# Kernel optimization log

Measured on AMD Instinct MI355X. Metric: run time of the kernel, lower is better.

The kernel has to match this reference:

```python
import jax, jax.numpy as jnp
import numpy as np

N_NODES = 100000
N_EDGES = 3200000
IN_DIM = 128
HID = 64


def setup_inputs() -> dict:
    key = jax.random.key(0)
    ks = jax.random.split(key, 12)
    x = jax.random.normal(ks[0], (N_NODES, IN_DIM), dtype=jnp.float32)
    edge_index = jax.random.randint(ks[1], (2, N_EDGES), 0, N_NODES, dtype=jnp.int64)
    batch = jnp.zeros((N_NODES,), dtype=jnp.int64)
    s = 0.05
    params = {
        'fc_W': jax.random.normal(ks[2], (HID, IN_DIM), jnp.float32) * s,
        'fc_b': jnp.zeros((HID,), jnp.float32),
        # SAGEConv layer 1: lin_l (neighbor aggr, has bias), lin_r (root)
        'Wl1': jax.random.normal(ks[3], (HID, HID), jnp.float32) * s,
        'bl1': jnp.zeros((HID,), jnp.float32),
        'Wr1': jax.random.normal(ks[4], (HID, HID), jnp.float32) * s,
        # SAGEConv layer 2
        'Wl2': jax.random.normal(ks[5], (HID, HID), jnp.float32) * s,
        'bl2': jnp.zeros((HID,), jnp.float32),
        'Wr2': jax.random.normal(ks[6], (HID, HID), jnp.float32) * s,
        'head_W': jax.random.normal(ks[7], (1, HID), jnp.float32) * s,
        'head_b': jnp.zeros((1,), jnp.float32),
    }
    return {'x': x, 'edge_index': edge_index, 'batch': batch, **params}


def _sage_conv(h, src, dst, Wl, bl, Wr, n_nodes):
    # mean-aggregate neighbor features: gather over src, scatter-sum to dst
    msgs = h[src]                                            # [E, HID]
    agg = jax.ops.segment_sum(msgs, dst, num_segments=n_nodes)
    deg = jax.ops.segment_sum(jnp.ones((src.shape[0],), h.dtype), dst,
                              num_segments=n_nodes)
    agg = agg / jnp.maximum(deg, 1.0)[:, None]               # mean aggr
    return agg @ Wl.T + bl + h @ Wr.T                        # lin_l + lin_r


def reference(x, edge_index, batch, fc_W, fc_b, Wl1, bl1, Wr1, Wl2, bl2, Wr2,
              head_W, head_b):
    n_nodes = x.shape[0]
    src, dst = edge_index[0], edge_index[1]
    h = jax.nn.relu(x @ fc_W.T + fc_b)                       # fc + relu
    h = jax.nn.relu(_sage_conv(h, src, dst, Wl1, bl1, Wr1, n_nodes))  # SAGE 1 + relu
    h = _sage_conv(h, src, dst, Wl2, bl2, Wr2, n_nodes)      # SAGE 2 (no act)
    return h @ head_W.T + head_b                             # head -> [N, 1]
```

## Files before the change

### kernel.cpp

```cpp
#include <hip/hip_runtime.h>

#define N_NODES 100000
#define N_EDGES 3200000
#define IN_DIM 128
#define HID 64

#define NPB 32
#define NBUCK 3125
#define NBUCKP 3328
#define NBUCKP2 4096
#define TILE 12800
#define NSEG 250
#define RAWCAP 1408
#define FCB 391

typedef __attribute__((ext_vector_type(8))) short short8;
typedef __attribute__((ext_vector_type(4))) float f32x4;
typedef __attribute__((ext_vector_type(2))) float f32x2;

__device__ inline float bf2f(unsigned short u) {
    union { unsigned int u; float f; } c;
    c.u = ((unsigned int)u) << 16;
    return c.f;
}
__device__ inline unsigned short f2bf(float f) {
    union { float f; unsigned int u; } c;
    c.f = f;
    unsigned int u = c.u;
    return (unsigned short)((u + 0x7fffu + ((u >> 16) & 1u)) >> 16);
}
__device__ inline short8 cvt8(const float* __restrict__ p) {
    f32x4 lo = *reinterpret_cast<const f32x4*>(p);
    f32x4 hi = *reinterpret_cast<const f32x4*>(p + 4);
    short8 r;
#pragma unroll
    for (int j = 0; j < 4; ++j) { r[j] = (short)f2bf(lo[j]); r[4 + j] = (short)f2bf(hi[j]); }
    return r;
}
__device__ inline unsigned short pk_f8(float a, float b) {
    return (unsigned short)(__builtin_amdgcn_cvt_pk_fp8_f32(a, b, 0, false) & 0xffff);
}

__global__ __launch_bounds__(1024) void pre_kernel(
    const float* __restrict__ x, const float* __restrict__ fcW,
    const float* __restrict__ fcb, unsigned short* __restrict__ h0,
    unsigned char* __restrict__ h0f8,
    const int* __restrict__ ei, unsigned int* __restrict__ stage,
    int* __restrict__ offs,
    const float* __restrict__ Wl1, const float* __restrict__ Wr1,
    const float* __restrict__ Wl2, const float* __restrict__ Wr2,
    unsigned short* __restrict__ Wbf) {
    __shared__ int hoff[NBUCKP2];
    __shared__ int wsum[16];
    int tid = threadIdx.x;
    int lane = tid & 63, wid = tid >> 6;

    if (blockIdx.x < FCB) {
        int wtile = blockIdx.x * 16 + wid;
        if (wtile >= N_NODES / 16) return;
        int col = lane & 15, quad = lane >> 4;
        short8 bw[4][4];
#pragma unroll
        for (int nt = 0; nt < 4; ++nt)
#pragma unroll
            for (int ks = 0; ks < 4; ++ks)
                bw[nt][ks] = cvt8(fcW + (nt * 16 + col) * IN_DIM + ks * 32 + quad * 8);
        f32x4 acc[4];
#pragma unroll
        for (int nt = 0; nt < 4; ++nt) acc[nt] = {0.f, 0.f, 0.f, 0.f};
        int node0 = wtile * 16;
        const float* xrow = x + (size_t)(node0 + col) * IN_DIM + quad * 8;
#pragma unroll
        for (int ks = 0; ks < 4; ++ks) {
            short8 a = cvt8(xrow + ks * 32);
#pragma unroll
            for (int nt = 0; nt < 4; ++nt)
                acc[nt] = __builtin_amdgcn_mfma_f32_16x16x32_bf16(a, bw[nt][ks], acc[nt], 0, 0, 0);
        }
#pragma unroll
        for (int nt = 0; nt < 4; ++nt) {
            float bias = fcb[nt * 16 + col];
#pragma unroll
            for (int r = 0; r < 4; ++r) {
                float v = acc[nt][r] + bias;
                v = v > 0.f ? v : 0.f;
                int node = node0 + quad * 4 + r;
                int f = nt * 16 + col;
                h0[(size_t)node * HID + f] = f2bf(v);
                float w = __shfl_xor(v, 1);
                if (!(col & 1))
                    *(unsigned short*)(h0f8 + (size_t)node * HID + f) = pk_f8(v, w);
            }
        }
    } else if (blockIdx.x < FCB + NSEG) {
        int blk = blockIdx.x - FCB;
        int e0 = blk * TILE;
        int sd[13], ss[13];
        for (int i = tid; i < NBUCKP2; i += 1024) hoff[i] = 0;
        __syncthreads();
#pragma unroll
        for (int k = 0; k < 13; ++k) {
            int i = tid + k * 1024;
            if (i < TILE) {
                sd[k] = ei[(size_t)N_EDGES + e0 + i];
                ss[k] = ei[e0 + i];
                atomicAdd(&hoff[sd[k] >> 5], 1);
            }
        }
        __syncthreads();
        int base = tid * 4;
        int vals[4];
        int s = 0;
#pragma unroll
        for (int j = 0; j < 4; ++j) { vals[j] = s; s += hoff[base + j]; }
        int inc = s;
#pragma unroll
        for (int d = 1; d < 64; d <<= 1) {
            int n = __shfl_up(inc, d);
            if (lane >= d) inc += n;
        }
        int wave_excl = inc - s;
        if (lane == 63) wsum[wid] = inc;
        __syncthreads();
        if (tid == 0) {
            int r = 0;
#pragma unroll
            for (int w = 0; w < 16; ++w) { int t = wsum[w]; wsum[w] = r; r += t; }
        }
        __syncthreads();
        int tbase = wsum[wid] + wave_excl;
        __syncthreads();
#pragma unroll
        for (int j = 0; j < 4; ++j) hoff[base + j] = tbase + vals[j];
        __syncthreads();
        int* og = offs + (size_t)blk * NBUCKP;
        for (int i = tid; i < NBUCKP; i += 1024) og[i] = hoff[i];
        __syncthreads();
        unsigned int* sg = stage + (size_t)blk * TILE;
#pragma unroll
        for (int k = 0; k < 13; ++k) {
            int i = tid + k * 1024;
            if (i < TILE) {
                int pos = atomicAdd(&hoff[sd[k] >> 5], 1);
                sg[pos] = ((unsigned int)ss[k] << 5) | (unsigned int)(sd[k] & 31);
            }
        }
    } else {
        const float* mats[4] = {Wl1, Wr1, Wl2, Wr2};
#pragma unroll
        for (int m = 0; m < 4; ++m)
            for (int i = tid; i < HID * HID; i += 1024)
                Wbf[m * HID * HID + i] = f2bf(mats[m][i]);
    }
}

__global__ __launch_bounds__(256) void agg_sage(
    const unsigned short* __restrict__ h, const unsigned char* __restrict__ h8,
    const unsigned int* __restrict__ stage, const int* __restrict__ offs,
    unsigned int* __restrict__ g_srt, int* __restrict__ g_cnt,
    const unsigned short* __restrict__ Wlb, const unsigned short* __restrict__ Wrb,
    const float* __restrict__ bl, const float* __restrict__ hw,
    const float* __restrict__ hbias,
    unsigned short* __restrict__ h_out, unsigned char* __restrict__ h8_out,
    float* __restrict__ head_out, int do_head, int mode) {
    __shared__ unsigned int raw[RAWCAP];
    __shared__ unsigned int srt[RAWCAP];
    __shared__ unsigned int aggT[NPB][36];
    __shared__ int cnt32[NPB], off32[NPB], pos32[NPB];
    __shared__ int seg_alloc;
    __shared__ float headacc[NPB];
    int tid = threadIdx.x;
    int lane = tid & 63, wid = tid >> 6;
    int b = blockIdx.x;

    if (mode == 0) {
        if (tid == 0) seg_alloc = 0;
        if (tid < NPB) { cnt32[tid] = 0; headacc[tid] = 0.f; }
        __syncthreads();
        if (tid < NSEG) {
            const int* ob = offs + (size_t)tid * NBUCKP + b;
            int s2 = ob[0], e2 = ob[1];
            int n = e2 - s2;
            if (n > 0) {
                int p = atomicAdd(&seg_alloc, n);
                if (p + n > RAWCAP) n = (RAWCAP > p) ? (RAWCAP - p) : 0;
                const unsigned int* sp = stage + (size_t)tid * TILE + s2;
                for (int i = 0; i < n; ++i) raw[p + i] = sp[i];
            }
        }
        __syncthreads();
        int total = seg_alloc;
        if (total > RAWCAP) total = RAWCAP;
        for (int i = tid; i < total; i += 256) atomicAdd(&cnt32[raw[i] & 31], 1);
        __syncthreads();
        if (tid == 0) {
            int r = 0;
            for (int j = 0; j < NPB; ++j) { off32[j] = r; pos32[j] = r; r += cnt32[j]; }
        }
        __syncthreads();
        for (int i = tid; i < total; i += 256) {
            unsigned int u = raw[i];
            int p = atomicAdd(&pos32[u & 31], 1);
            srt[p] = u >> 5;
        }
        __syncthreads();
        for (int i = tid; i < total; i += 256) g_srt[(size_t)b * RAWCAP + i] = srt[i];
        if (tid < NPB) {
            g_cnt[b * 64 + tid] = cnt32[tid];
            g_cnt[b * 64 + 32 + tid] = off32[tid];
        }
    } else {
        if (tid < NPB) {
            cnt32[tid] = g_cnt[b * 64 + tid];
            off32[tid] = g_cnt[b * 64 + 32 + tid];
            headacc[tid] = 0.f;
        }
        __syncthreads();
        int total = off32[NPB - 1] + cnt32[NPB - 1];
        for (int i = tid; i < total; i += 256) srt[i] = g_srt[(size_t)b * RAWCAP + i];
        __syncthreads();
    }

    int q = lane >> 4, f4 = lane & 15;
#pragma unroll
    for (int k = 0; k < 8; ++k) {
        int d = wid * 8 + k;
        int s = off32[d], n = cnt32[d];
        float a0 = 0.f, a1 = 0.f, a2 = 0.f, a3 = 0.f;
        int i = 0;
        for (; i + 32 <= n; i += 32) {
            unsigned int g[8];
#pragma unroll
            for (int j = 0; j < 8; ++j) {
                unsigned int e = srt[s + i + j * 4 + q];
                g[j] = *(const unsigned int*)(h8 + (size_t)e * HID + f4 * 4);
            }
#pragma unroll
            for (int j = 0; j < 8; ++j) {
                f32x2 lo = __builtin_amdgcn_cvt_pk_f32_fp8(g[j], false);
                f32x2 hi = __builtin_amdgcn_cvt_pk_f32_fp8(g[j], true);
                a0 += lo.x; a1 += lo.y; a2 += hi.x; a3 += hi.y;
            }
        }
        for (; i + 16 <= n; i += 16) {
            unsigned int g[4];
#pragma unroll
            for (int j = 0; j < 4; ++j) {
                unsigned int e = srt[s + i + j * 4 + q];
                g[j] = *(const unsigned int*)(h8 + (size_t)e * HID + f4 * 4);
            }
#pragma unroll
            for (int j = 0; j < 4; ++j) {
                f32x2 lo = __builtin_amdgcn_cvt_pk_f32_fp8(g[j], false);
                f32x2 hi = __builtin_amdgcn_cvt_pk_f32_fp8(g[j], true);
                a0 += lo.x; a1 += lo.y; a2 += hi.x; a3 += hi.y;
            }
        }
        for (; i < n; i += 4) {
            int valid = (i + q) < n;
            unsigned int e = srt[valid ? (s + i + q) : s];
            unsigned int g = *(const unsigned int*)(h8 + (size_t)e * HID + f4 * 4);
            if (valid) {
                f32x2 lo = __builtin_amdgcn_cvt_pk_f32_fp8(g, false);
                f32x2 hi = __builtin_amdgcn_cvt_pk_f32_fp8(g, true);
                a0 += lo.x; a1 += lo.y; a2 += hi.x; a3 += hi.y;
            }
        }
        a0 += __shfl_xor(a0, 16); a0 += __shfl_xor(a0, 32);
        a1 += __shfl_xor(a1, 16); a1 += __shfl_xor(a1, 32);
        a2 += __shfl_xor(a2, 16); a2 += __shfl_xor(a2, 32);
        a3 += __shfl_xor(a3, 16); a3 += __shfl_xor(a3, 32);
        if (q == 0) {
            float inv = n > 0 ? 1.f / (float)n : 0.f;
            aggT[d][f4 * 2] = (unsigned int)f2bf(a0 * inv) |
                              ((unsigned int)f2bf(a1 * inv) << 16);
            aggT[d][f4 * 2 + 1] = (unsigned int)f2bf(a2 * inv) |
                                  ((unsigned int)f2bf(a3 * inv) << 16);
        }
    }
    __syncthreads();

    {
        int t = wid >> 1, np = wid & 1;
        int col = lane & 15, quad = lane >> 4;
        int m = t * 16 + col;
        int node0 = b * NPB;

        short8 aggA[2], hinA[2];
        const unsigned short* aggrow = (const unsigned short*)&aggT[m][0];
#pragma unroll
        for (int ks = 0; ks < 2; ++ks) {
            aggA[ks] = *reinterpret_cast<const short8*>(aggrow + ks * 32 + quad * 8);
            hinA[ks] = *reinterpret_cast<const short8*>(
                h + (size_t)(node0 + m) * HID + ks * 32 + quad * 8);
        }
        short8 bwl[2][2], bwr[2][2];
#pragma unroll
        for (int nt = 0; nt < 2; ++nt) {
            int f = np * 32 + nt * 16 + col;
#pragma unroll
            for (int ks = 0; ks < 2; ++ks) {
                bwl[nt][ks] = *reinterpret_cast<const short8*>(
                    Wlb + (size_t)f * HID + ks * 32 + quad * 8);
                bwr[nt][ks] = *reinterpret_cast<const short8*>(
                    Wrb + (size_t)f * HID + ks * 32 + quad * 8);
            }
        }
        f32x4 acc[2];
#pragma unroll
        for (int nt = 0; nt < 2; ++nt) acc[nt] = {0.f, 0.f, 0.f, 0.f};
#pragma unroll
        for (int ks = 0; ks < 2; ++ks) {
#pragma unroll
            for (int nt = 0; nt < 2; ++nt) {
                acc[nt] = __builtin_amdgcn_mfma_f32_16x16x32_bf16(aggA[ks], bwl[nt][ks], acc[nt], 0, 0, 0);
                acc[nt] = __builtin_amdgcn_mfma_f32_16x16x32_bf16(hinA[ks], bwr[nt][ks], acc[nt], 0, 0, 0);
            }
        }

        if (!do_head) {
#pragma unroll
            for (int nt = 0; nt < 2; ++nt) {
                int f = np * 32 + nt * 16 + col;
                float bias = bl[f];
#pragma unroll
                for (int r = 0; r < 4; ++r) {
                    float v = acc[nt][r] + bias;
                    v = v > 0.f ? v : 0.f;
                    int node = node0 + t * 16 + quad * 4 + r;
                    h_out[(size_t)node * HID + f] = f2bf(v);
                    float w = __shfl_xor(v, 1);
                    if (!(col & 1))
                        *(unsigned short*)(h8_out + (size_t)node * HID + f) = pk_f8(v, w);
                }
            }
        } else {
            float vr[4] = {0.f, 0.f, 0.f, 0.f};
#pragma unroll
            for (int nt = 0; nt < 2; ++nt) {
                int f = np * 32 + nt * 16 + col;
                float w = hw[f], bias = bl[f];
#pragma unroll
                for (int r = 0; r < 4; ++r) vr[r] += (acc[nt][r] + bias) * w;
            }
#pragma unroll
            for (int r = 0; r < 4; ++r) {
#pragma unroll
                for (int d = 1; d < 16; d <<= 1) vr[r] += __shfl_xor(vr[r], d);
            }
            if (col == 0) {
#pragma unroll
                for (int r = 0; r < 4; ++r)
                    atomicAdd(&headacc[t * 16 + quad * 4 + r], vr[r]);
            }
            __syncthreads();
            if (tid < NPB) head_out[node0 + tid] = headacc[tid] + hbias[0];
        }
    }
}

extern "C" void kernel_launch(void* const* d_in, const int* in_sizes, int n_in,
                              void* d_out, int out_size, void* d_ws, size_t ws_size,
                              hipStream_t stream) {
    const float* x   = (const float*)d_in[0];
    const int*   ei  = (const int*)d_in[1];
    const float* fcW = (const float*)d_in[3];
    const float* fcb = (const float*)d_in[4];
    const float* Wl1 = (const float*)d_in[5];
    const float* bl1 = (const float*)d_in[6];
    const float* Wr1 = (const float*)d_in[7];
    const float* Wl2 = (const float*)d_in[8];
    const float* bl2 = (const float*)d_in[9];
    const float* Wr2 = (const float*)d_in[10];
    const float* hW  = (const float*)d_in[11];
    const float* hb  = (const float*)d_in[12];
    float* out = (float*)d_out;

    char* ws = (char*)d_ws;
    size_t off = 0;
    auto alloc = [&](size_t bytes) -> char* {
        char* p = ws + off;
        off = (off + bytes + 255) & ~(size_t)255;
        return p;
    };
    unsigned short* h0   = (unsigned short*)alloc((size_t)N_NODES * HID * 2);
    unsigned short* h1   = (unsigned short*)alloc((size_t)N_NODES * HID * 2);
    unsigned char*  h0f8 = (unsigned char*)alloc((size_t)N_NODES * HID);
    unsigned char*  h1f8 = (unsigned char*)alloc((size_t)N_NODES * HID);
    unsigned int* stage  = (unsigned int*)alloc((size_t)N_EDGES * 4);
    int* offs            = (int*)alloc((size_t)NSEG * NBUCKP * 4);
    unsigned int* g_srt  = (unsigned int*)alloc((size_t)NBUCK * RAWCAP * 4);
    int* g_cnt           = (int*)alloc((size_t)NBUCK * 64 * 4);
    unsigned short* Wbf  = (unsigned short*)alloc((size_t)4 * HID * HID * 2);

    pre_kernel<<<FCB + NSEG + 1, 1024, 0, stream>>>(
        x, fcW, fcb, h0, h0f8, ei, stage, offs, Wl1, Wr1, Wl2, Wr2, Wbf);
    agg_sage<<<NBUCK, 256, 0, stream>>>(h0, h0f8, stage, offs, g_srt, g_cnt,
                                        Wbf, Wbf + HID * HID, bl1,
                                        nullptr, nullptr, h1, h1f8, nullptr, 0, 0);
    agg_sage<<<NBUCK, 256, 0, stream>>>(h1, h1f8, stage, offs, g_srt, g_cnt,
                                        Wbf + 2 * HID * HID, Wbf + 3 * HID * HID, bl2,
                                        hW, hb, nullptr, nullptr, out, 1, 1);
}
```

Before: 293.8 us.

## Partition neighbor gathers into source-node quarters for L2 locality across blocks

Within each destination bucket, edges are now sorted by (destination, source-quarter), and the gather loop runs over four source-range passes, accumulating partial sums in shared memory reused from the raw edge buffer. The aim is that blocks running concurrently touch the same quarter of the fp8 feature table at the same time, which should improve L2/MALL hit rates for the random gathers. In exchange, each destination's segments are split into shorter runs with less unrolling, there are extra shared-memory read-modify-writes, and the count metadata grows to 129 offsets per block.

```diff
diff --git a/kernel.cpp b/kernel.cpp
--- a/kernel.cpp
+++ b/kernel.cpp
@@ -13,6 +13,8 @@
 #define NSEG 250
 #define RAWCAP 1408
 #define FCB 391
+#define NQT 4
+#define CNT_STRIDE 132
 
 typedef __attribute__((ext_vector_type(8))) short short8;
 typedef __attribute__((ext_vector_type(4))) float f32x4;
@@ -39,6 +41,9 @@
 }
 __device__ inline unsigned short pk_f8(float a, float b) {
     return (unsigned short)(__builtin_amdgcn_cvt_pk_fp8_f32(a, b, 0, false) & 0xffff);
+}
+__device__ inline unsigned int src_qt(unsigned int s) {
+    return (s * 42950u) >> 30;
 }
 
 __global__ __launch_bounds__(1024) void pre_kernel(
@@ -154,6 +159,11 @@
     }
 }
 
+union __align__(16) RawAgg {
+    unsigned int raw[RAWCAP];
+    float aggF[NPB][64];
+};
+
 __global__ __launch_bounds__(256) void agg_sage(
     const unsigned short* __restrict__ h, const unsigned char* __restrict__ h8,
     const unsigned int* __restrict__ stage, const int* __restrict__ offs,
@@ -163,10 +173,12 @@
     const float* __restrict__ hbias,
     unsigned short* __restrict__ h_out, unsigned char* __restrict__ h8_out,
     float* __restrict__ head_out, int do_head, int mode) {
-    __shared__ unsigned int raw[RAWCAP];
+    __shared__ RawAgg u_;
     __shared__ unsigned int srt[RAWCAP];
     __shared__ unsigned int aggT[NPB][36];
-    __shared__ int cnt32[NPB], off32[NPB], pos32[NPB];
+    __shared__ int off129[129];
+    __shared__ int cnt128[128];
+    __shared__ int pos128[128];
     __shared__ int seg_alloc;
     __shared__ float headacc[NPB];
     int tid = threadIdx.x;
@@ -175,7 +187,8 @@
 
     if (mode == 0) {
         if (tid == 0) seg_alloc = 0;
-        if (tid < NPB) { cnt32[tid] = 0; headacc[tid] = 0.f; }
+        for (int i = tid; i < 128; i += 256) cnt128[i] = 0;
+        if (tid < NPB) headacc[tid] = 0.f;
         __syncthreads();
         if (tid < NSEG) {
             const int* ob = offs + (size_t)tid * NBUCKP + b;
@@ -185,97 +198,119 @@
                 int p = atomicAdd(&seg_alloc, n);
                 if (p + n > RAWCAP) n = (RAWCAP > p) ? (RAWCAP - p) : 0;
                 const unsigned int* sp = stage + (size_t)tid * TILE + s2;
-                for (int i = 0; i < n; ++i) raw[p + i] = sp[i];
+                for (int i = 0; i < n; ++i) u_.raw[p + i] = sp[i];
             }
         }
         __syncthreads();
         int total = seg_alloc;
         if (total > RAWCAP) total = RAWCAP;
-        for (int i = tid; i < total; i += 256) atomicAdd(&cnt32[raw[i] & 31], 1);
+        for (int i = tid; i < total; i += 256) {
+            unsigned int u = u_.raw[i];
+            int key = (int)(((u & 31u) << 2) | src_qt(u >> 5));
+            atomicAdd(&cnt128[key], 1);
+        }
         __syncthreads();
         if (tid == 0) {
             int r = 0;
-            for (int j = 0; j < NPB; ++j) { off32[j] = r; pos32[j] = r; r += cnt32[j]; }
+            for (int j = 0; j < 128; ++j) { off129[j] = r; pos128[j] = r; r += cnt128[j]; }
+            off129[128] = r;
         }
         __syncthreads();
         for (int i = tid; i < total; i += 256) {
-            unsigned int u = raw[i];
-            int p = atomicAdd(&pos32[u & 31], 1);
-            srt[p] = u >> 5;
+            unsigned int u = u_.raw[i];
+            unsigned int s = u >> 5;
+            int key = (int)(((u & 31u) << 2) | src_qt(s));
+            int p = atomicAdd(&pos128[key], 1);
+            srt[p] = s;
         }
         __syncthreads();
         for (int i = tid; i < total; i += 256) g_srt[(size_t)b * RAWCAP + i] = srt[i];
-        if (tid < NPB) {
-            g_cnt[b * 64 + tid] = cnt32[tid];
-            g_cnt[b * 64 + 32 + tid] = off32[tid];
-        }
+        if (tid < 129) g_cnt[b * CNT_STRIDE + tid] = off129[tid];
     } else {
-        if (tid < NPB) {
-            cnt32[tid] = g_cnt[b * 64 + tid];
-            off32[tid] = g_cnt[b * 64 + 32 + tid];
-            headacc[tid] = 0.f;
-        }
-        __syncthreads();
-        int total = off32[NPB - 1] + cnt32[NPB - 1];
+        for (int i = tid; i < 129; i += 256) off129[i] = g_cnt[b * CNT_STRIDE + i];
+        if (tid < NPB) headacc[tid] = 0.f;
+        __syncthreads();
+        int total = off129[128];
         for (int i = tid; i < total; i += 256) srt[i] = g_srt[(size_t)b * RAWCAP + i];
         __syncthreads();
     }
 
     int q = lane >> 4, f4 = lane & 15;
+#pragma unroll 1
+    for (int qt = 0; qt < NQT; ++qt) {
+#pragma unroll
+        for (int k = 0; k < 8; ++k) {
+            int d = wid * 8 + k;
+            int s = off129[(d << 2) + qt];
+            int n = off129[(d << 2) + qt + 1] - s;
+            float a0 = 0.f, a1 = 0.f, a2 = 0.f, a3 = 0.f;
+            int i = 0;
+            for (; i + 16 <= n; i += 16) {
+                unsigned int g[4];
+#pragma unroll
+                for (int j = 0; j < 4; ++j) {
+                    unsigned int e = srt[s + i + j * 4 + q];
+                    g[j] = *(const unsigned int*)(h8 + (size_t)e * HID + f4 * 4);
+                }
+#pragma unroll
+                for (int j = 0; j < 4; ++j) {
+                    f32x2 lo = __builtin_amdgcn_cvt_pk_f32_fp8(g[j], false);
+                    f32x2 hi = __builtin_amdgcn_cvt_pk_f32_fp8(g[j], true);
+                    a0 += lo.x; a1 += lo.y; a2 += hi.x; a3 += hi.y;
+                }
+            }
+            for (; i + 8 <= n; i += 8) {
+                unsigned int g[2];
+#pragma unroll
+                for (int j = 0; j < 2; ++j) {
+                    unsigned int e = srt[s + i + j * 4 + q];
+                    g[j] = *(const unsigned int*)(h8 + (size_t)e * HID + f4 * 4);
+                }
+#pragma unroll
+                for (int j = 0; j < 2; ++j) {
+                    f32x2 lo = __builtin_amdgcn_cvt_pk_f32_fp8(g[j], false);
+                    f32x2 hi = __builtin_amdgcn_cvt_pk_f32_fp8(g[j], true);
+                    a0 += lo.x; a1 += lo.y; a2 += hi.x; a3 += hi.y;
+                }
+            }
+            for (; i < n; i += 4) {
+                int valid = (i + q) < n;
+                unsigned int e = srt[valid ? (s + i + q) : s];
+                unsigned int g = *(const unsigned int*)(h8 + (size_t)e * HID + f4 * 4);
+                if (valid) {
+                    f32x2 lo = __builtin_amdgcn_cvt_pk_f32_fp8(g, false);
+                    f32x2 hi = __builtin_amdgcn_cvt_pk_f32_fp8(g, true);
+                    a0 += lo.x; a1 += lo.y; a2 += hi.x; a3 += hi.y;
+                }
+            }
+            a0 += __shfl_xor(a0, 16); a0 += __shfl_xor(a0, 32);
+            a1 += __shfl_xor(a1, 16); a1 += __shfl_xor(a1, 32);
+            a2 += __shfl_xor(a2, 16); a2 += __shfl_xor(a2, 32);
+            a3 += __shfl_xor(a3, 16); a3 += __shfl_xor(a3, 32);
+            if (q == 0) {
+                f32x4* p = (f32x4*)&u_.aggF[d][f4 * 4];
+                if (qt == 0) {
+                    f32x4 v = {a0, a1, a2, a3};
+                    *p = v;
+                } else {
+                    f32x4 v = *p;
+                    v[0] += a0; v[1] += a1; v[2] += a2; v[3] += a3;
+                    *p = v;
+                }
+            }
+        }
+    }
 #pragma unroll
     for (int k = 0; k < 8; ++k) {
         int d = wid * 8 + k;
-        int s = off32[d], n = cnt32[d];
-        float a0 = 0.f, a1 = 0.f, a2 = 0.f, a3 = 0.f;
-        int i = 0;
-        for (; i + 32 <= n; i += 32) {
-            unsigned int g[8];
-#pragma unroll
-            for (int j = 0; j < 8; ++j) {
-                unsigned int e = srt[s + i + j * 4 + q];
-                g[j] = *(const unsigned int*)(h8 + (size_t)e * HID + f4 * 4);
-            }
-#pragma unroll
-            for (int j = 0; j < 8; ++j) {
-                f32x2 lo = __builtin_amdgcn_cvt_pk_f32_fp8(g[j], false);
-                f32x2 hi = __builtin_amdgcn_cvt_pk_f32_fp8(g[j], true);
-                a0 += lo.x; a1 += lo.y; a2 += hi.x; a3 += hi.y;
-            }
-        }
-        for (; i + 16 <= n; i += 16) {
-            unsigned int g[4];
-#pragma unroll
-            for (int j = 0; j < 4; ++j) {
-                unsigned int e = srt[s + i + j * 4 + q];
-                g[j] = *(const unsigned int*)(h8 + (size_t)e * HID + f4 * 4);
-            }
-#pragma unroll
-            for (int j = 0; j < 4; ++j) {
-                f32x2 lo = __builtin_amdgcn_cvt_pk_f32_fp8(g[j], false);
-                f32x2 hi = __builtin_amdgcn_cvt_pk_f32_fp8(g[j], true);
-                a0 += lo.x; a1 += lo.y; a2 += hi.x; a3 += hi.y;
-            }
-        }
-        for (; i < n; i += 4) {
-            int valid = (i + q) < n;
-            unsigned int e = srt[valid ? (s + i + q) : s];
-            unsigned int g = *(const unsigned int*)(h8 + (size_t)e * HID + f4 * 4);
-            if (valid) {
-                f32x2 lo = __builtin_amdgcn_cvt_pk_f32_fp8(g, false);
-                f32x2 hi = __builtin_amdgcn_cvt_pk_f32_fp8(g, true);
-                a0 += lo.x; a1 += lo.y; a2 += hi.x; a3 += hi.y;
-            }
-        }
-        a0 += __shfl_xor(a0, 16); a0 += __shfl_xor(a0, 32);
-        a1 += __shfl_xor(a1, 16); a1 += __shfl_xor(a1, 32);
-        a2 += __shfl_xor(a2, 16); a2 += __shfl_xor(a2, 32);
-        a3 += __shfl_xor(a3, 16); a3 += __shfl_xor(a3, 32);
         if (q == 0) {
-            float inv = n > 0 ? 1.f / (float)n : 0.f;
-            aggT[d][f4 * 2] = (unsigned int)f2bf(a0 * inv) |
-                              ((unsigned int)f2bf(a1 * inv) << 16);
-            aggT[d][f4 * 2 + 1] = (unsigned int)f2bf(a2 * inv) |
-                                  ((unsigned int)f2bf(a3 * inv) << 16);
+            int nT = off129[(d << 2) + 4] - off129[d << 2];
+            float inv = nT > 0 ? 1.f / (float)nT : 0.f;
+            f32x4 v = *(f32x4*)&u_.aggF[d][f4 * 4];
+            aggT[d][f4 * 2] = (unsigned int)f2bf(v[0] * inv) |
+                              ((unsigned int)f2bf(v[1] * inv) << 16);
+            aggT[d][f4 * 2 + 1] = (unsigned int)f2bf(v[2] * inv) |
+                                  ((unsigned int)f2bf(v[3] * inv) << 16);
         }
     }
     __syncthreads();
@@ -390,7 +425,7 @@
     unsigned int* stage  = (unsigned int*)alloc((size_t)N_EDGES * 4);
     int* offs            = (int*)alloc((size_t)NSEG * NBUCKP * 4);
     unsigned int* g_srt  = (unsigned int*)alloc((size_t)NBUCK * RAWCAP * 4);
-    int* g_cnt           = (int*)alloc((size_t)NBUCK * 64 * 4);
+    int* g_cnt           = (int*)alloc((size_t)NBUCK * CNT_STRIDE * 4);
     unsigned short* Wbf  = (unsigned short*)alloc((size_t)4 * HID * HID * 2);
 
     pre_kernel<<<FCB + NSEG + 1, 1024, 0, stream>>>(
```

After: 358.5 us. 1.22x slower.

## Split fp8 feature tables into two 32-wide halves and aggregate each in separate passes

Applied to the files above, without the earlier changes.

Stores the fp8 node features as two separate planes, features 0-31 and 32-63, so each table is 3.2MB instead of 6.4MB. Each SAGE layer now runs two aggregation launches: phase 0 gathers the low half and writes partial bf16 means to a global buffer, and phase 1 gathers the high half, reloads the low half and runs the MFMA transform. The goal is for each gather pass's working set to fit better in L2/MALL and to cut cache misses on the random gathers. The cost is twice the launches, another pass over the sorted edge lists per layer, and extra global traffic for the partial aggregates.

```diff
diff --git a/kernel.cpp b/kernel.cpp
--- a/kernel.cpp
+++ b/kernel.cpp
@@ -18,11 +18,6 @@
 typedef __attribute__((ext_vector_type(4))) float f32x4;
 typedef __attribute__((ext_vector_type(2))) float f32x2;
 
-__device__ inline float bf2f(unsigned short u) {
-    union { unsigned int u; float f; } c;
-    c.u = ((unsigned int)u) << 16;
-    return c.f;
-}
 __device__ inline unsigned short f2bf(float f) {
     union { float f; unsigned int u; } c;
     c.f = f;
@@ -44,7 +39,7 @@
 __global__ __launch_bounds__(1024) void pre_kernel(
     const float* __restrict__ x, const float* __restrict__ fcW,
     const float* __restrict__ fcb, unsigned short* __restrict__ h0,
-    unsigned char* __restrict__ h0f8,
+    unsigned char* __restrict__ h0lo, unsigned char* __restrict__ h0hi,
     const int* __restrict__ ei, unsigned int* __restrict__ stage,
     int* __restrict__ offs,
     const float* __restrict__ Wl1, const float* __restrict__ Wr1,
@@ -80,6 +75,8 @@
 #pragma unroll
         for (int nt = 0; nt < 4; ++nt) {
             float bias = fcb[nt * 16 + col];
+            unsigned char* pl = (nt >> 1) ? h0hi : h0lo;
+            int fp = (nt & 1) * 16 + col;
 #pragma unroll
             for (int r = 0; r < 4; ++r) {
                 float v = acc[nt][r] + bias;
@@ -89,7 +86,7 @@
                 h0[(size_t)node * HID + f] = f2bf(v);
                 float w = __shfl_xor(v, 1);
                 if (!(col & 1))
-                    *(unsigned short*)(h0f8 + (size_t)node * HID + f) = pk_f8(v, w);
+                    *(unsigned short*)(pl + (size_t)node * 32 + fp) = pk_f8(v, w);
             }
         }
     } else if (blockIdx.x < FCB + NSEG) {
@@ -155,14 +152,16 @@
 }
 
 __global__ __launch_bounds__(256) void agg_sage(
-    const unsigned short* __restrict__ h, const unsigned char* __restrict__ h8,
+    const unsigned short* __restrict__ h, const unsigned char* __restrict__ pl8,
     const unsigned int* __restrict__ stage, const int* __restrict__ offs,
     unsigned int* __restrict__ g_srt, int* __restrict__ g_cnt,
+    unsigned int* __restrict__ aggLo,
     const unsigned short* __restrict__ Wlb, const unsigned short* __restrict__ Wrb,
     const float* __restrict__ bl, const float* __restrict__ hw,
     const float* __restrict__ hbias,
-    unsigned short* __restrict__ h_out, unsigned char* __restrict__ h8_out,
-    float* __restrict__ head_out, int do_head, int mode) {
+    unsigned short* __restrict__ h_out, unsigned char* __restrict__ h8lo_out,
+    unsigned char* __restrict__ h8hi_out,
+    float* __restrict__ head_out, int do_head, int mode, int phase) {
     __shared__ unsigned int raw[RAWCAP];
     __shared__ unsigned int srt[RAWCAP];
     __shared__ unsigned int aggT[NPB][36];
@@ -221,70 +220,92 @@
         __syncthreads();
     }
 
-    int q = lane >> 4, f4 = lane & 15;
-#pragma unroll
-    for (int k = 0; k < 8; ++k) {
-        int d = wid * 8 + k;
-        int s = off32[d], n = cnt32[d];
-        float a0 = 0.f, a1 = 0.f, a2 = 0.f, a3 = 0.f;
-        int i = 0;
-        for (; i + 32 <= n; i += 32) {
-            unsigned int g[8];
-#pragma unroll
-            for (int j = 0; j < 8; ++j) {
-                unsigned int e = srt[s + i + j * 4 + q];
-                g[j] = *(const unsigned int*)(h8 + (size_t)e * HID + f4 * 4);
-            }
-#pragma unroll
-            for (int j = 0; j < 8; ++j) {
-                f32x2 lo = __builtin_amdgcn_cvt_pk_f32_fp8(g[j], false);
-                f32x2 hi = __builtin_amdgcn_cvt_pk_f32_fp8(g[j], true);
-                a0 += lo.x; a1 += lo.y; a2 += hi.x; a3 += hi.y;
-            }
-        }
-        for (; i + 16 <= n; i += 16) {
-            unsigned int g[4];
-#pragma unroll
-            for (int j = 0; j < 4; ++j) {
-                unsigned int e = srt[s + i + j * 4 + q];
-                g[j] = *(const unsigned int*)(h8 + (size_t)e * HID + f4 * 4);
-            }
-#pragma unroll
-            for (int j = 0; j < 4; ++j) {
-                f32x2 lo = __builtin_amdgcn_cvt_pk_f32_fp8(g[j], false);
-                f32x2 hi = __builtin_amdgcn_cvt_pk_f32_fp8(g[j], true);
-                a0 += lo.x; a1 += lo.y; a2 += hi.x; a3 += hi.y;
-            }
-        }
-        for (; i < n; i += 4) {
-            int valid = (i + q) < n;
-            unsigned int e = srt[valid ? (s + i + q) : s];
-            unsigned int g = *(const unsigned int*)(h8 + (size_t)e * HID + f4 * 4);
-            if (valid) {
-                f32x2 lo = __builtin_amdgcn_cvt_pk_f32_fp8(g, false);
-                f32x2 hi = __builtin_amdgcn_cvt_pk_f32_fp8(g, true);
-                a0 += lo.x; a1 += lo.y; a2 += hi.x; a3 += hi.y;
-            }
-        }
-        a0 += __shfl_xor(a0, 16); a0 += __shfl_xor(a0, 32);
-        a1 += __shfl_xor(a1, 16); a1 += __shfl_xor(a1, 32);
-        a2 += __shfl_xor(a2, 16); a2 += __shfl_xor(a2, 32);
-        a3 += __shfl_xor(a3, 16); a3 += __shfl_xor(a3, 32);
-        if (q == 0) {
-            float inv = n > 0 ? 1.f / (float)n : 0.f;
-            aggT[d][f4 * 2] = (unsigned int)f2bf(a0 * inv) |
-                              ((unsigned int)f2bf(a1 * inv) << 16);
-            aggT[d][f4 * 2 + 1] = (unsigned int)f2bf(a2 * inv) |
-                                  ((unsigned int)f2bf(a3 * inv) << 16);
-        }
+    int node0 = b * NPB;
+
+    if (phase == 1) {
+        int d = tid >> 3, c = tid & 7;
+        aggT[d][c] = aggLo[(size_t)(node0 + d) * 16 + c];
+        aggT[d][c + 8] = aggLo[(size_t)(node0 + d) * 16 + c + 8];
     }
+
+    {
+        int o = lane >> 3, fo4 = lane & 7;
+        unsigned int fo = (unsigned int)(fo4 * 4);
+#pragma unroll
+        for (int k = 0; k < 8; ++k) {
+            int d = wid * 8 + k;
+            int s = off32[d], n = cnt32[d];
+            f32x2 A0 = {0.f, 0.f}, A1 = {0.f, 0.f};
+            int i = 0;
+            for (; i + 32 <= n; i += 32) {
+                unsigned int g[4];
+#pragma unroll
+                for (int j = 0; j < 4; ++j) {
+                    unsigned int e = srt[s + i + j * 8 + o];
+                    g[j] = *(const unsigned int*)(pl8 + e * 32u + fo);
+                }
+#pragma unroll
+                for (int j = 0; j < 4; ++j) {
+                    A0 += __builtin_amdgcn_cvt_pk_f32_fp8(g[j], false);
+                    A1 += __builtin_amdgcn_cvt_pk_f32_fp8(g[j], true);
+                }
+            }
+            for (; i + 16 <= n; i += 16) {
+                unsigned int g[2];
+#pragma unroll
+                for (int j = 0; j < 2; ++j) {
+                    unsigned int e = srt[s + i + j * 8 + o];
+                    g[j] = *(const unsigned int*)(pl8 + e * 32u + fo);
+                }
+#pragma unroll
+                for (int j = 0; j < 2; ++j) {
+                    A0 += __builtin_amdgcn_cvt_pk_f32_fp8(g[j], false);
+                    A1 += __builtin_amdgcn_cvt_pk_f32_fp8(g[j], true);
+                }
+            }
+            for (; i + 8 <= n; i += 8) {
+                unsigned int e = srt[s + i + o];
+                unsigned int g = *(const unsigned int*)(pl8 + e * 32u + fo);
+                A0 += __builtin_amdgcn_cvt_pk_f32_fp8(g, false);
+                A1 += __builtin_amdgcn_cvt_pk_f32_fp8(g, true);
+            }
+            if (i < n) {
+                int valid = (i + o) < n;
+                unsigned int e = srt[valid ? (s + i + o) : s];
+                unsigned int g = *(const unsigned int*)(pl8 + e * 32u + fo);
+                if (valid) {
+                    A0 += __builtin_amdgcn_cvt_pk_f32_fp8(g, false);
+                    A1 += __builtin_amdgcn_cvt_pk_f32_fp8(g, true);
+                }
+            }
+#pragma unroll
+            for (int dl = 8; dl < 64; dl <<= 1) {
+                A0.x += __shfl_xor(A0.x, dl); A0.y += __shfl_xor(A0.y, dl);
+                A1.x += __shfl_xor(A1.x, dl); A1.y += __shfl_xor(A1.y, dl);
+            }
+            if (o == 0) {
+                float inv = n > 0 ? 1.f / (float)n : 0.f;
+                unsigned int w0 = (unsigned int)f2bf(A0.x * inv) |
+                                  ((unsigned int)f2bf(A0.y * inv) << 16);
+                unsigned int w1 = (unsigned int)f2bf(A1.x * inv) |
+                                  ((unsigned int)f2bf(A1.y * inv) << 16);
+                if (phase == 0) {
+                    aggLo[(size_t)(node0 + d) * 16 + fo4 * 2] = w0;
+                    aggLo[(size_t)(node0 + d) * 16 + fo4 * 2 + 1] = w1;
+                } else {
+                    aggT[d][16 + fo4 * 2] = w0;
+                    aggT[d][16 + fo4 * 2 + 1] = w1;
+                }
+            }
+        }
+    }
+    if (phase == 0) return;
     __syncthreads();
 
     {
         int t = wid >> 1, np = wid & 1;
         int col = lane & 15, quad = lane >> 4;
         int m = t * 16 + col;
-        int node0 = b * NPB;
 
         short8 aggA[2], hinA[2];
         const unsigned short* aggrow = (const unsigned short*)&aggT[m][0];
@@ -319,9 +340,11 @@
         }
 
         if (!do_head) {
+            unsigned char* pl = np ? h8hi_out : h8lo_out;
 #pragma unroll
             for (int nt = 0; nt < 2; ++nt) {
                 int f = np * 32 + nt * 16 + col;
+                int fp = nt * 16 + col;
                 float bias = bl[f];
 #pragma unroll
                 for (int r = 0; r < 4; ++r) {
@@ -331,7 +354,7 @@
                     h_out[(size_t)node * HID + f] = f2bf(v);
                     float w = __shfl_xor(v, 1);
                     if (!(col & 1))
-                        *(unsigned short*)(h8_out + (size_t)node * HID + f) = pk_f8(v, w);
+                        *(unsigned short*)(pl + (size_t)node * 32 + fp) = pk_f8(v, w);
                 }
             }
         } else {
@@ -385,20 +408,33 @@
     };
     unsigned short* h0   = (unsigned short*)alloc((size_t)N_NODES * HID * 2);
     unsigned short* h1   = (unsigned short*)alloc((size_t)N_NODES * HID * 2);
-    unsigned char*  h0f8 = (unsigned char*)alloc((size_t)N_NODES * HID);
-    unsigned char*  h1f8 = (unsigned char*)alloc((size_t)N_NODES * HID);
+    unsigned char*  h0lo = (unsigned char*)alloc((size_t)N_NODES * 32);
+    unsigned char*  h0hi = (unsigned char*)alloc((size_t)N_NODES * 32);
+    unsigned char*  h1lo = (unsigned char*)alloc((size_t)N_NODES * 32);
+    unsigned char*  h1hi = (unsigned char*)alloc((size_t)N_NODES * 32);
     unsigned int* stage  = (unsigned int*)alloc((size_t)N_EDGES * 4);
     int* offs            = (int*)alloc((size_t)NSEG * NBUCKP * 4);
     unsigned int* g_srt  = (unsigned int*)alloc((size_t)NBUCK * RAWCAP * 4);
     int* g_cnt           = (int*)alloc((size_t)NBUCK * 64 * 4);
+    unsigned int* aggLo  = (unsigned int*)alloc((size_t)N_NODES * 64);
     unsigned short* Wbf  = (unsigned short*)alloc((size_t)4 * HID * HID * 2);
 
     pre_kernel<<<FCB + NSEG + 1, 1024, 0, stream>>>(
-        x, fcW, fcb, h0, h0f8, ei, stage, offs, Wl1, Wr1, Wl2, Wr2, Wbf);
-    agg_sage<<<NBUCK, 256, 0, stream>>>(h0, h0f8, stage, offs, g_srt, g_cnt,
+        x, fcW, fcb, h0, h0lo, h0hi, ei, stage, offs, Wl1, Wr1, Wl2, Wr2, Wbf);
+    agg_sage<<<NBUCK, 256, 0, stream>>>(h0, h0lo, stage, offs, g_srt, g_cnt, aggLo,
                                         Wbf, Wbf + HID * HID, bl1,
-                                        nullptr, nullptr, h1, h1f8, nullptr, 0, 0);
-    agg_sage<<<NBUCK, 256, 0, stream>>>(h1, h1f8, stage, offs, g_srt, g_cnt,
+                                        nullptr, nullptr, h1, h1lo, h1hi,
+                                        nullptr, 0, 0, 0);
+    agg_sage<<<NBUCK, 256, 0, stream>>>(h0, h0hi, stage, offs, g_srt, g_cnt, aggLo,
+                                        Wbf, Wbf + HID * HID, bl1,
+                                        nullptr, nullptr, h1, h1lo, h1hi,
+                                        nullptr, 0, 1, 1);
+    agg_sage<<<NBUCK, 256, 0, stream>>>(h1, h1lo, stage, offs, g_srt, g_cnt, aggLo,
                                         Wbf + 2 * HID * HID, Wbf + 3 * HID * HID, bl2,
-                                        hW, hb, nullptr, nullptr, out, 1, 1);
-}
+                                        hW, hb, nullptr, nullptr, nullptr,
+                                        nullptr, 0, 1, 0);
+    agg_sage<<<NBUCK, 256, 0, stream>>>(h1, h1hi, stage, offs, g_srt, g_cnt, aggLo,
+                                        Wbf + 2 * HID * HID, Wbf + 3 * HID * HID, bl2,
+                                        hW, hb, nullptr, nullptr, nullptr,
+                                        out, 1, 1, 1);
+}
```

New measurement: 332.6 us. 13.2% more time.
